# Optimization experiments

Measured on AMD Instinct MI355X. Metric: run time of the kernel, lower is better.

Reference implementation:

```python
import math
import jax, jax.numpy as jnp
import numpy as np

B, S, H, D = 2, 2048, 16, 64

def setup_inputs() -> dict:
    key = jax.random.key(0)
    kq, kk, kv = jax.random.split(key, 3)
    query = jax.random.normal(kq, (B, S, H, D), dtype=jnp.float32)
    k_ = jax.random.normal(kk, (B, S, H, D), dtype=jnp.float32)
    v_ = jax.random.normal(kv, (B, S, H, D), dtype=jnp.float32)
    return {"query": query, "key": k_, "value": v_}

def reference(query, key, value):
    # USPAttention.__call__ with req=None -> simple_attention, causal=False
    scale = 1.0 / math.sqrt(query.shape[-1])
    q = jnp.transpose(query, (0, 2, 1, 3))  # [B,H,S,D]
    k = jnp.transpose(key, (0, 2, 1, 3))
    v = jnp.transpose(value, (0, 2, 1, 3))
    attn = jnp.einsum('bhsd,bhtd->bhst', q, k) * scale  # [B,H,S,S]
    attn = jax.nn.softmax(attn, axis=-1)
    out = jnp.einsum('bhst,bhtd->bhsd', attn, v)
    return jnp.transpose(out, (0, 2, 1, 3))  # [B,S,H,D]
```

## Files before the change

kernel.cpp:

```cpp
#include <hip/hip_runtime.h>
#include <hip/hip_bf16.h>
#include <math.h>

typedef float f32x4 __attribute__((ext_vector_type(4)));
typedef short s16x8 __attribute__((ext_vector_type(8)));

#define NS 2048
#define NH 16
#define ND 64
#define QTILE 128
#define KVB 64
#define NT (NS / KVB)
#define L2E 1.44269504f

__device__ __forceinline__ unsigned short f2bf(float f) {
    union { float f; unsigned u; } c; c.f = f;
    return (unsigned short)((c.u + 0x7FFFu + ((c.u >> 16) & 1u)) >> 16);
}
__device__ __forceinline__ unsigned pack2bf(float a, float b) {
    return (unsigned)f2bf(a) | ((unsigned)f2bf(b) << 16);
}

__global__ __launch_bounds__(512, 4)
void usp_attn(const float* __restrict__ Qg, const float* __restrict__ Kg,
              const float* __restrict__ Vg, float* __restrict__ Og) {
    __shared__ unsigned short Klds[2][64 * 64];
    __shared__ unsigned short Vt[2][64 * 64];
    __shared__ unsigned short Plds[8][16 * 64];

    const int tid  = threadIdx.x;
    const int w    = tid >> 6;
    const int lane = tid & 63;
    const int g    = lane >> 4;
    const int x    = lane & 15;

    int bid = blockIdx.x;
    int wg  = (bid & 7) * 64 + (bid >> 3);
    int qt  = wg & 15;
    int bh  = wg >> 4;
    int b   = bh >> 4;
    int h   = bh & 15;
    int q0  = qt * QTILE;

    const int srow = NH * ND;
    const size_t base = ((size_t)b * NS * NH + h) * ND;

    const int qrow = q0 + w * 16 + x;
    const float* qp = Qg + base + (size_t)qrow * srow;
    s16x8 qf[2];
#pragma unroll
    for (int ks = 0; ks < 2; ++ks) {
        int d0 = ks * 32 + g * 8;
        f32x4 a = *(const f32x4*)(qp + d0);
        f32x4 c = *(const f32x4*)(qp + d0 + 4);
        union { s16x8 v; unsigned u[4]; } r;
        r.u[0] = pack2bf(a[0] * 0.125f, a[1] * 0.125f);
        r.u[1] = pack2bf(a[2] * 0.125f, a[3] * 0.125f);
        r.u[2] = pack2bf(c[0] * 0.125f, c[1] * 0.125f);
        r.u[3] = pack2bf(c[2] * 0.125f, c[3] * 0.125f);
        qf[ks] = r.v;
    }

    f32x4 oacc[4];
#pragma unroll
    for (int dt = 0; dt < 4; ++dt) oacc[dt] = f32x4{0.f, 0.f, 0.f, 0.f};
    float mrun = -INFINITY, lrun = 0.f;

    const int sub = tid >> 4;
    const int c4  = (tid & 15) * 4;
    const float* kb = Kg + base + (size_t)sub * srow + c4;
    const float* vb = Vg + base + (size_t)sub * srow + c4;

    f32x4 kreg[2], vreg[2];
#define LOADT(t) do { \
        size_t off = (size_t)(t) * KVB * srow; \
        kreg[0] = *(const f32x4*)(kb + off); \
        kreg[1] = *(const f32x4*)(kb + off + (size_t)32 * srow); \
        vreg[0] = *(const f32x4*)(vb + off); \
        vreg[1] = *(const f32x4*)(vb + off + (size_t)32 * srow); \
    } while (0)

#define STORET(bf) do { \
        _Pragma("unroll") \
        for (int p = 0; p < 2; ++p) { \
            int kv = sub + 32 * p; \
            int de = c4 ^ ((kv & 7) << 3); \
            *(uint2*)(&Klds[bf][kv * 64 + de]) = \
                uint2{pack2bf(kreg[p][0], kreg[p][1]), pack2bf(kreg[p][2], kreg[p][3])}; \
            _Pragma("unroll") \
            for (int i = 0; i < 4; ++i) { \
                int d = c4 + i; \
                Vt[bf][d * 64 + (kv ^ (((d >> 1) & 7) << 3))] = f2bf(vreg[p][i]); \
            } \
        } \
    } while (0)

    LOADT(0);
    STORET(0);
    LOADT(1);
    __syncthreads();

    unsigned short* Pw = &Plds[w][0];
    const int rsw = (x & 7) << 3;
    const int vsw = (x >> 1) << 3;

    for (int t = 0; t < NT; ++t) {
        const unsigned short* Kc = &Klds[t & 1][0];
        const unsigned short* Vc = &Vt[t & 1][0];

        if (t + 1 < NT) STORET((t + 1) & 1);
        if (t + 2 < NT) LOADT(t + 2);

        f32x4 sc[4];
#pragma unroll
        for (int nt = 0; nt < 4; ++nt) sc[nt] = f32x4{0.f, 0.f, 0.f, 0.f};
        __builtin_amdgcn_s_setprio(1);
#pragma unroll
        for (int nt = 0; nt < 4; ++nt) {
            int krow = (16 * nt + x) * 64;
#pragma unroll
            for (int ks = 0; ks < 2; ++ks) {
                s16x8 kf = *(const s16x8*)(&Kc[krow + ((32 * ks + 8 * g) ^ rsw)]);
                sc[nt] = __builtin_amdgcn_mfma_f32_16x16x32_bf16(kf, qf[ks], sc[nt], 0, 0, 0);
            }
        }
        __builtin_amdgcn_s_setprio(0);

        float mx = sc[0][0];
#pragma unroll
        for (int nt = 0; nt < 4; ++nt)
#pragma unroll
            for (int r = 0; r < 4; ++r) mx = fmaxf(mx, sc[nt][r]);
        mx = fmaxf(mx, __shfl_xor(mx, 16));
        mx = fmaxf(mx, __shfl_xor(mx, 32));
        float mnew = fmaxf(mrun, mx);
        float alpha = exp2f((mrun - mnew) * L2E);
        float rs = 0.f;
#pragma unroll
        for (int nt = 0; nt < 4; ++nt) {
#pragma unroll
            for (int r = 0; r < 4; ++r) {
                float p = exp2f((sc[nt][r] - mnew) * L2E);
                sc[nt][r] = p;
                rs += p;
            }
            *(uint2*)(&Pw[x * 64 + ((16 * nt + 4 * g) ^ rsw)]) =
                uint2{pack2bf(sc[nt][0], sc[nt][1]), pack2bf(sc[nt][2], sc[nt][3])};
        }
        rs += __shfl_xor(rs, 16);
        rs += __shfl_xor(rs, 32);
        lrun = lrun * alpha + rs;
        mrun = mnew;
#pragma unroll
        for (int dt = 0; dt < 4; ++dt)
#pragma unroll
            for (int r = 0; r < 4; ++r) oacc[dt][r] *= alpha;

        __builtin_amdgcn_s_setprio(1);
#pragma unroll
        for (int ks = 0; ks < 2; ++ks) {
            int k0 = 32 * ks + 8 * g;
            s16x8 pf = *(const s16x8*)(&Pw[x * 64 + (k0 ^ rsw)]);
#pragma unroll
            for (int dt = 0; dt < 4; ++dt) {
                s16x8 vf = *(const s16x8*)(&Vc[(16 * dt + x) * 64 + (k0 ^ vsw)]);
                oacc[dt] = __builtin_amdgcn_mfma_f32_16x16x32_bf16(vf, pf, oacc[dt], 0, 0, 0);
            }
        }
        __builtin_amdgcn_s_setprio(0);

        __syncthreads();
    }

    float inv = 1.0f / lrun;
    float* op = Og + base + (size_t)qrow * srow;
#pragma unroll
    for (int dt = 0; dt < 4; ++dt) {
        f32x4 r = oacc[dt];
        r[0] *= inv; r[1] *= inv; r[2] *= inv; r[3] *= inv;
        *(f32x4*)(op + 16 * dt + 4 * g) = r;
    }
}

extern "C" void kernel_launch(void* const* d_in, const int* in_sizes, int n_in,
                              void* d_out, int out_size, void* d_ws, size_t ws_size,
                              hipStream_t stream) {
    const float* Q = (const float*)d_in[0];
    const float* K = (const float*)d_in[1];
    const float* V = (const float*)d_in[2];
    float* O = (float*)d_out;
    usp_attn<<<dim3(512), dim3(512), 0, stream>>>(Q, K, V, O);
}
```

Before: 170.6 us.

## Fold log2e into Q scale, defer softmax rescale, use hardware bf16 pack

Folds the log2(e) factor into the Q pre-scale so the exponentials need no extra multiply. Online-softmax rescaling of the running max and accumulators is skipped unless some lane's new max exceeds the running max by more than a threshold. The manual bit-twiddling bf16 rounding is replaced with the v_cvt_pk_bf16_f32 instruction, and the V transpose store packs two elements per conversion. Together these aim to cut VALU work in the softmax and in LDS staging. The deferred rescale lets exponent values grow up to about 2^11.5 before rebasing, which risks bf16 precision loss in P if the threshold is too loose.

```diff
diff --git a/kernel.cpp b/kernel.cpp
--- a/kernel.cpp
+++ b/kernel.cpp
@@ -11,14 +11,13 @@
 #define QTILE 128
 #define KVB 64
 #define NT (NS / KVB)
-#define L2E 1.44269504f
+#define QSCALE 0.18033688f
+#define DEFER_THR 11.5f
 
-__device__ __forceinline__ unsigned short f2bf(float f) {
-    union { float f; unsigned u; } c; c.f = f;
-    return (unsigned short)((c.u + 0x7FFFu + ((c.u >> 16) & 1u)) >> 16);
-}
-__device__ __forceinline__ unsigned pack2bf(float a, float b) {
-    return (unsigned)f2bf(a) | ((unsigned)f2bf(b) << 16);
+__device__ __forceinline__ unsigned cvtpk(float lo, float hi) {
+    unsigned r;
+    asm("v_cvt_pk_bf16_f32 %0, %1, %2" : "=v"(r) : "v"(lo), "v"(hi));
+    return r;
 }
 
 __global__ __launch_bounds__(512, 4)
@@ -54,10 +53,10 @@
         f32x4 a = *(const f32x4*)(qp + d0);
         f32x4 c = *(const f32x4*)(qp + d0 + 4);
         union { s16x8 v; unsigned u[4]; } r;
-        r.u[0] = pack2bf(a[0] * 0.125f, a[1] * 0.125f);
-        r.u[1] = pack2bf(a[2] * 0.125f, a[3] * 0.125f);
-        r.u[2] = pack2bf(c[0] * 0.125f, c[1] * 0.125f);
-        r.u[3] = pack2bf(c[2] * 0.125f, c[3] * 0.125f);
+        r.u[0] = cvtpk(a[0] * QSCALE, a[1] * QSCALE);
+        r.u[1] = cvtpk(a[2] * QSCALE, a[3] * QSCALE);
+        r.u[2] = cvtpk(c[0] * QSCALE, c[1] * QSCALE);
+        r.u[3] = cvtpk(c[2] * QSCALE, c[3] * QSCALE);
         qf[ks] = r.v;
     }
 
@@ -86,12 +85,15 @@
             int kv = sub + 32 * p; \
             int de = c4 ^ ((kv & 7) << 3); \
             *(uint2*)(&Klds[bf][kv * 64 + de]) = \
-                uint2{pack2bf(kreg[p][0], kreg[p][1]), pack2bf(kreg[p][2], kreg[p][3])}; \
-            _Pragma("unroll") \
-            for (int i = 0; i < 4; ++i) { \
-                int d = c4 + i; \
-                Vt[bf][d * 64 + (kv ^ (((d >> 1) & 7) << 3))] = f2bf(vreg[p][i]); \
-            } \
+                uint2{cvtpk(kreg[p][0], kreg[p][1]), cvtpk(kreg[p][2], kreg[p][3])}; \
+            unsigned va = cvtpk(vreg[p][0], vreg[p][1]); \
+            unsigned vb2 = cvtpk(vreg[p][2], vreg[p][3]); \
+            int s01 = kv ^ (((c4 >> 1) & 7) << 3); \
+            int s23 = kv ^ ((((c4 >> 1) + 1) & 7) << 3); \
+            Vt[bf][(c4 + 0) * 64 + s01] = (unsigned short)va; \
+            Vt[bf][(c4 + 1) * 64 + s01] = (unsigned short)(va >> 16); \
+            Vt[bf][(c4 + 2) * 64 + s23] = (unsigned short)vb2; \
+            Vt[bf][(c4 + 3) * 64 + s23] = (unsigned short)(vb2 >> 16); \
         } \
     } while (0)
 
@@ -133,28 +135,30 @@
             for (int r = 0; r < 4; ++r) mx = fmaxf(mx, sc[nt][r]);
         mx = fmaxf(mx, __shfl_xor(mx, 16));
         mx = fmaxf(mx, __shfl_xor(mx, 32));
-        float mnew = fmaxf(mrun, mx);
-        float alpha = exp2f((mrun - mnew) * L2E);
+        if (!__all(mx - mrun <= DEFER_THR)) {
+            float mnew = fmaxf(mrun, mx);
+            float alpha = exp2f(mrun - mnew);
+            mrun = mnew;
+            lrun *= alpha;
+#pragma unroll
+            for (int dt = 0; dt < 4; ++dt)
+#pragma unroll
+                for (int r = 0; r < 4; ++r) oacc[dt][r] *= alpha;
+        }
         float rs = 0.f;
 #pragma unroll
         for (int nt = 0; nt < 4; ++nt) {
-#pragma unroll
-            for (int r = 0; r < 4; ++r) {
-                float p = exp2f((sc[nt][r] - mnew) * L2E);
-                sc[nt][r] = p;
-                rs += p;
-            }
+            float p0 = exp2f(sc[nt][0] - mrun);
+            float p1 = exp2f(sc[nt][1] - mrun);
+            float p2 = exp2f(sc[nt][2] - mrun);
+            float p3 = exp2f(sc[nt][3] - mrun);
+            rs += (p0 + p1) + (p2 + p3);
             *(uint2*)(&Pw[x * 64 + ((16 * nt + 4 * g) ^ rsw)]) =
-                uint2{pack2bf(sc[nt][0], sc[nt][1]), pack2bf(sc[nt][2], sc[nt][3])};
+                uint2{cvtpk(p0, p1), cvtpk(p2, p3)};
         }
         rs += __shfl_xor(rs, 16);
         rs += __shfl_xor(rs, 32);
-        lrun = lrun * alpha + rs;
-        mrun = mnew;
-#pragma unroll
-        for (int dt = 0; dt < 4; ++dt)
-#pragma unroll
-            for (int r = 0; r < 4; ++r) oacc[dt][r] *= alpha;
+        lrun += rs;
 
         __builtin_amdgcn_s_setprio(1);
 #pragma unroll
```

Measured after the change: 153.9 us. -9.8%, faster.
